# Optimization experiments

Measured on AMD Instinct MI355X. Metric: run time of the kernel, lower is better.

Reference implementation:

```python
import jax, jax.numpy as jnp
import numpy as np

B = 2048      # graphs per side
NPG = 40      # nodes per graph
N = B * NPG   # 81920 total nodes
E = 4 * N     # 327680 directed edges
IN_DIM = 74
H = 256
ADD = 8
GCR_LAYERS = 5
MLP1, MLP2 = 1024, 512


def setup_inputs() -> dict:
    key = jax.random.key(0)
    ks = jax.random.split(key, 24)
    n2g = jnp.repeat(jnp.arange(B, dtype=jnp.int32), NPG)
    s = 0.05
    d = {
        'cat_src': jax.random.randint(ks[0], (E,), 0, N, dtype=jnp.int32),
        'cat_dst': jax.random.randint(ks[1], (E,), 0, N, dtype=jnp.int32),
        'cat_n2g': n2g,
        'cat_x': jax.random.normal(ks[2], (N, IN_DIM), jnp.float32),
        'an_src': jax.random.randint(ks[3], (E,), 0, N, dtype=jnp.int32),
        'an_dst': jax.random.randint(ks[4], (E,), 0, N, dtype=jnp.int32),
        'an_n2g': n2g,
        'an_x': jax.random.normal(ks[5], (N, IN_DIM), jnp.float32),
        'add_features': jax.random.normal(ks[6], (B, ADD), jnp.float32),
        # shared GNN params (same module processes cation and anion)
        'W0': jax.random.normal(ks[7], (IN_DIM, H), jnp.float32) * s,
        'b0': jnp.zeros((H,), jnp.float32),
        'gcrW': jax.random.normal(ks[8], (GCR_LAYERS, 2, H, H), jnp.float32) * s,
        'gcrb': jnp.zeros((GCR_LAYERS, 2, H), jnp.float32),
        # MLP head: (2H + ADD) -> 1024 -> 512 -> 1
        'mW1': jax.random.normal(ks[9], (2 * H + ADD, MLP1), jnp.float32) * s,
        'mb1': jnp.zeros((MLP1,), jnp.float32),
        'mW2': jax.random.normal(ks[10], (MLP1, MLP2), jnp.float32) * s,
        'mb2': jnp.zeros((MLP2,), jnp.float32),
        'mW3': jax.random.normal(ks[11], (MLP2, 1), jnp.float32) * s,
        'mb3': jnp.zeros((1,), jnp.float32),
    }
    return d


def _graph_conv(src, dst, x, W, b):
    # DGL GraphConv, norm='both': out = D_in^{-1/2} A^T D_out^{-1/2} x W + b
    ones = jnp.ones(src.shape[0], x.dtype)
    deg_out = jnp.clip(jax.ops.segment_sum(ones, src, num_segments=N), 1.0)
    deg_in = jnp.clip(jax.ops.segment_sum(ones, dst, num_segments=N), 1.0)
    h = x * jax.lax.rsqrt(deg_out)[:, None]
    agg = jax.ops.segment_sum(h[src], dst, num_segments=N)  # [N, d]
    return (agg * jax.lax.rsqrt(deg_in)[:, None]) @ W + b


def _feat_extract(src, dst, n2g, x, W0, b0, gcrW, gcrb):
    h = _graph_conv(src, dst, x, W0, b0)  # no activation after first conv
    for i in range(GCR_LAYERS):
        o1 = _graph_conv(src, dst, h, gcrW[i, 0], gcrb[i, 0])
        o2 = _graph_conv(src, dst, jax.nn.relu(o1), gcrW[i, 1], gcrb[i, 1])
        h = jax.nn.relu(o2)  # res_connection = 0 -> plain replace
    # dgl.sum_nodes readout per graph
    return jax.ops.segment_sum(h, n2g, num_segments=B)  # [B, H]


def _leaky(x):
    return jnp.where(x > 0, x, 0.01 * x)  # nn.LeakyReLU default slope


def reference(cat_src, cat_dst, cat_n2g, cat_x, an_src, an_dst, an_n2g, an_x,
              add_features, W0, b0, gcrW, gcrb, mW1, mb1, mW2, mb2, mW3, mb3):
    cat_feat = _feat_extract(cat_src, cat_dst, cat_n2g, cat_x, W0, b0, gcrW, gcrb)
    an_feat = _feat_extract(an_src, an_dst, an_n2g, an_x, W0, b0, gcrW, gcrb)
    z = jnp.concatenate([cat_feat, an_feat, add_features], axis=1)  # [B, 2H+ADD]
    h = _leaky(z @ mW1 + mb1)
    h = _leaky(h @ mW2 + mb2)
    out = h @ mW3 + mb3  # [B, 1]
    return out.squeeze(-1)
```

## Files before the change

kernel.cpp:

```cpp
#include <hip/hip_runtime.h>


#define NN 81920
#define NN2 163840
#define NE 327680
#define NE2 655360
#define NB 2048
#define NB2 4096
#define H 256
#define INDIM 74
#define KPAD 128
#define ZK 576
#define DEGCAP 32
#define CPITCH 132

typedef unsigned short u16;
typedef __attribute__((ext_vector_type(8))) short short8;
typedef __attribute__((ext_vector_type(4))) float f32x4;

__device__ inline u16 f2b(float f) {
    unsigned u = __builtin_bit_cast(unsigned, f);
    u += 0x7fffu + ((u >> 16) & 1u);
    return (u16)(u >> 16);
}
__device__ inline float b2f(u16 b) {
    unsigned u = ((unsigned)b) << 16;
    return __builtin_bit_cast(float, u);
}
__device__ inline float blo(unsigned u) { return __builtin_bit_cast(float, u << 16); }
__device__ inline float bhi(unsigned u) { return __builtin_bit_cast(float, u & 0xffff0000u); }

__global__ void fill_kernel(const int* __restrict__ cs, const int* __restrict__ cd,
                            const int* __restrict__ as_, const int* __restrict__ ad,
                            int* __restrict__ dego, int* __restrict__ cnti,
                            int* __restrict__ bucket) {
    int e = blockIdx.x * 256 + threadIdx.x;
    if (e < NE2) {
        int s, d;
        if (e < NE) { s = cs[e]; d = cd[e]; }
        else        { s = as_[e - NE] + NN; d = ad[e - NE] + NN; }
        atomicAdd(&dego[s], 1);
        int p = atomicAdd(&cnti[d], 1);
        if (p < DEGCAP) bucket[(size_t)p * NN2 + d] = s;
    }
}

__global__ void rsqrt_kernel(const int* __restrict__ dego, const int* __restrict__ cnti,
                             float* __restrict__ rso, float* __restrict__ rsi) {
    int i = blockIdx.x * 256 + threadIdx.x;
    if (i < NN2) {
        rso[i] = rsqrtf((float)(dego[i] > 1 ? dego[i] : 1));
        rsi[i] = rsqrtf((float)(cnti[i] > 1 ? cnti[i] : 1));
    }
}

__global__ __launch_bounds__(256) void prescale_x_kernel(
        const float* __restrict__ cx, const float* __restrict__ ax,
        const float* __restrict__ rso, u16* __restrict__ xbp) {
    int t = threadIdx.x;
    int node = blockIdx.x * 4 + (t >> 6);
    int lane = t & 63;
    const float* x = (node < NN) ? (cx + (size_t)node * INDIM)
                                 : (ax + (size_t)(node - NN) * INDIM);
    float w = rso[node];
    int f0 = lane * 2, f1 = f0 + 1;
    u16 a = (f0 < INDIM) ? f2b(x[f0] * w) : (u16)0;
    u16 b = (f1 < INDIM) ? f2b(x[f1] * w) : (u16)0;
    ((unsigned*)xbp)[(size_t)node * 64 + lane] = a | ((unsigned)b << 16);
}

__global__ __launch_bounds__(256) void gather_x_kernel(
        const u16* __restrict__ xbp, const int* __restrict__ bucket,
        const int* __restrict__ cnti, const float* __restrict__ rsi,
        u16* __restrict__ out) {
    int node = blockIdx.x * 16 + (threadIdx.x >> 4);
    int fc = (threadIdx.x & 15) * 8;
    int deg = cnti[node]; if (deg > DEGCAP) deg = DEGCAP;
    const int* bk = bucket + node;
    float acc[8] = {};
    for (int base = 0; base < deg; base += 4) {
        int i0 = bk[(size_t)base * NN2];
        int i1 = (base + 1 < deg) ? bk[(size_t)(base + 1) * NN2] : i0;
        int i2 = (base + 2 < deg) ? bk[(size_t)(base + 2) * NN2] : i0;
        int i3 = (base + 3 < deg) ? bk[(size_t)(base + 3) * NN2] : i0;
        float m1 = (base + 1 < deg) ? 1.f : 0.f;
        float m2 = (base + 2 < deg) ? 1.f : 0.f;
        float m3 = (base + 3 < deg) ? 1.f : 0.f;
        uint4 v0 = *(const uint4*)(xbp + (size_t)i0 * KPAD + fc);
        uint4 v1 = *(const uint4*)(xbp + (size_t)i1 * KPAD + fc);
        uint4 v2 = *(const uint4*)(xbp + (size_t)i2 * KPAD + fc);
        uint4 v3 = *(const uint4*)(xbp + (size_t)i3 * KPAD + fc);
        acc[0] += blo(v0.x) + m1 * blo(v1.x) + m2 * blo(v2.x) + m3 * blo(v3.x);
        acc[1] += bhi(v0.x) + m1 * bhi(v1.x) + m2 * bhi(v2.x) + m3 * bhi(v3.x);
        acc[2] += blo(v0.y) + m1 * blo(v1.y) + m2 * blo(v2.y) + m3 * blo(v3.y);
        acc[3] += bhi(v0.y) + m1 * bhi(v1.y) + m2 * bhi(v2.y) + m3 * bhi(v3.y);
        acc[4] += blo(v0.z) + m1 * blo(v1.z) + m2 * blo(v2.z) + m3 * blo(v3.z);
        acc[5] += bhi(v0.z) + m1 * bhi(v1.z) + m2 * bhi(v2.z) + m3 * bhi(v3.z);
        acc[6] += blo(v0.w) + m1 * blo(v1.w) + m2 * blo(v2.w) + m3 * blo(v3.w);
        acc[7] += bhi(v0.w) + m1 * bhi(v1.w) + m2 * bhi(v2.w) + m3 * bhi(v3.w);
    }
    float ri = rsi[node];
    u16 o[8];
#pragma unroll
    for (int i = 0; i < 8; ++i) o[i] = f2b(acc[i] * ri);
    uint4 ov;
    ov.x = o[0] | ((unsigned)o[1] << 16);
    ov.y = o[2] | ((unsigned)o[3] << 16);
    ov.z = o[4] | ((unsigned)o[5] << 16);
    ov.w = o[6] | ((unsigned)o[7] << 16);
    *(uint4*)(out + (size_t)node * KPAD + fc) = ov;
}

__global__ __launch_bounds__(256) void gather_h_kernel(
        const u16* __restrict__ h, const int* __restrict__ bucket,
        const int* __restrict__ cnti, const float* __restrict__ rso,
        const float* __restrict__ rsi, u16* __restrict__ out) {
    int node = blockIdx.x * 8 + (threadIdx.x >> 5);
    int fc = (threadIdx.x & 31) * 8;
    int deg = cnti[node]; if (deg > DEGCAP) deg = DEGCAP;
    const int* bk = bucket + node;
    float acc[8] = {};
    for (int base = 0; base < deg; base += 4) {
        int i0 = bk[(size_t)base * NN2];
        int i1 = (base + 1 < deg) ? bk[(size_t)(base + 1) * NN2] : i0;
        int i2 = (base + 2 < deg) ? bk[(size_t)(base + 2) * NN2] : i0;
        int i3 = (base + 3 < deg) ? bk[(size_t)(base + 3) * NN2] : i0;
        float w0 = rso[i0];
        float w1 = (base + 1 < deg) ? rso[i1] : 0.f;
        float w2 = (base + 2 < deg) ? rso[i2] : 0.f;
        float w3 = (base + 3 < deg) ? rso[i3] : 0.f;
        uint4 v0 = *(const uint4*)(h + (size_t)i0 * H + fc);
        uint4 v1 = *(const uint4*)(h + (size_t)i1 * H + fc);
        uint4 v2 = *(const uint4*)(h + (size_t)i2 * H + fc);
        uint4 v3 = *(const uint4*)(h + (size_t)i3 * H + fc);
        acc[0] += blo(v0.x) * w0 + blo(v1.x) * w1 + blo(v2.x) * w2 + blo(v3.x) * w3;
        acc[1] += bhi(v0.x) * w0 + bhi(v1.x) * w1 + bhi(v2.x) * w2 + bhi(v3.x) * w3;
        acc[2] += blo(v0.y) * w0 + blo(v1.y) * w1 + blo(v2.y) * w2 + blo(v3.y) * w3;
        acc[3] += bhi(v0.y) * w0 + bhi(v1.y) * w1 + bhi(v2.y) * w2 + bhi(v3.y) * w3;
        acc[4] += blo(v0.z) * w0 + blo(v1.z) * w1 + blo(v2.z) * w2 + blo(v3.z) * w3;
        acc[5] += bhi(v0.z) * w0 + bhi(v1.z) * w1 + bhi(v2.z) * w2 + bhi(v3.z) * w3;
        acc[6] += blo(v0.w) * w0 + blo(v1.w) * w1 + blo(v2.w) * w2 + blo(v3.w) * w3;
        acc[7] += bhi(v0.w) * w0 + bhi(v1.w) * w1 + bhi(v2.w) * w2 + bhi(v3.w) * w3;
    }
    float ri = rsi[node];
    u16 o[8];
#pragma unroll
    for (int i = 0; i < 8; ++i) o[i] = f2b(acc[i] * ri);
    uint4 ov;
    ov.x = o[0] | ((unsigned)o[1] << 16);
    ov.y = o[2] | ((unsigned)o[3] << 16);
    ov.z = o[4] | ((unsigned)o[5] << 16);
    ov.w = o[6] | ((unsigned)o[7] << 16);
    *(uint4*)(out + (size_t)node * H + fc) = ov;
}

__global__ void prep_w0_kernel(const float* __restrict__ W0, u16* __restrict__ Wt0) {
    int i = blockIdx.x * 256 + threadIdx.x;
    int n = i >> 7, k = i & 127;
    float v = (k < INDIM) ? W0[(size_t)k * H + n] : 0.f;
    Wt0[i] = f2b(v);
}

__global__ void prep_gcr_kernel(const float* __restrict__ W, u16* __restrict__ Wt) {
    int i = blockIdx.x * 256 + threadIdx.x;
    int l = blockIdx.y;
    int n = i >> 8, k = i & 255;
    Wt[(size_t)l * 65536 + i] = f2b(W[(size_t)l * 65536 + (size_t)k * H + n]);
}

__global__ void prep_w1_kernel(const float* __restrict__ W, u16* __restrict__ Wt) {
    int i = blockIdx.x * 256 + threadIdx.x;
    if (i >= 1024 * ZK) return;
    int n = i / ZK, k = i - n * ZK;
    float v = (k < 520) ? W[(size_t)k * 1024 + n] : 0.f;
    Wt[i] = f2b(v);
}

__global__ void prep_w2_kernel(const float* __restrict__ W, u16* __restrict__ Wt) {
    int i = blockIdx.x * 256 + threadIdx.x;
    int n = i >> 10, k = i & 1023;
    Wt[i] = f2b(W[(size_t)k * 512 + n]);
}

__device__ inline void ldg_lds16(const u16* g, u16* l) {
    __builtin_amdgcn_global_load_lds(
        (const __attribute__((address_space(1))) unsigned int*)g,
        (__attribute__((address_space(3))) unsigned int*)l, 16, 0, 0);
}
__device__ inline float actf(float v, int act) {
    if (act == 1) return fmaxf(v, 0.f);
    if (act == 2) return (v > 0.f) ? v : 0.01f * v;
    return v;
}

__global__ __launch_bounds__(256) void gemm_mfma_kernel(
        const u16* __restrict__ A, int lda,
        const u16* __restrict__ Bt, int ldb,
        const float* __restrict__ bias, u16* __restrict__ C, int ldc,
        int Kiters, int act) {
    __shared__ __align__(16) u16 smem[128 * CPITCH];
    u16* As = smem;
    u16* Bs = smem + 8192;
    int t = threadIdx.x;
    int wave = t >> 6, lane = t & 63;
    int wr = wave >> 1, wc = wave & 1;
    int row0 = blockIdx.y * 128, col0 = blockIdx.x * 128;

    int sr = t >> 3;
    int ksrc = (((t & 7) ^ (sr & 7))) * 8;
    const u16* Ag[4];
    const u16* Bg[4];
#pragma unroll
    for (int c = 0; c < 4; ++c) {
        Ag[c] = A + (size_t)(row0 + c * 32 + sr) * lda + ksrc;
        Bg[c] = Bt + (size_t)(col0 + c * 32 + sr) * ldb + ksrc;
    }
    u16* AsW = As + wave * 512;
    u16* BsW = Bs + wave * 512;

    f32x4 acc[4][4] = {};
    int mrow = lane & 15;
    int q = lane >> 4;

    for (int kt = 0; kt < Kiters; ++kt) {
#pragma unroll
        for (int c = 0; c < 4; ++c) ldg_lds16(Ag[c], AsW + c * 2048);
#pragma unroll
        for (int c = 0; c < 4; ++c) ldg_lds16(Bg[c], BsW + c * 2048);
        __syncthreads();
#pragma unroll
        for (int kk = 0; kk < 2; ++kk) {
            short8 a[4], b[4];
#pragma unroll
            for (int mt = 0; mt < 4; ++mt) {
                int row = wr * 64 + mt * 16 + mrow;
                int seg = (kk * 4 + q) ^ (row & 7);
                a[mt] = *(const short8*)(As + row * 64 + seg * 8);
            }
#pragma unroll
            for (int nt = 0; nt < 4; ++nt) {
                int row = wc * 64 + nt * 16 + mrow;
                int seg = (kk * 4 + q) ^ (row & 7);
                b[nt] = *(const short8*)(Bs + row * 64 + seg * 8);
            }
#pragma unroll
            for (int mt = 0; mt < 4; ++mt)
#pragma unroll
                for (int nt = 0; nt < 4; ++nt)
                    acc[mt][nt] = __builtin_amdgcn_mfma_f32_16x16x32_bf16(
                        a[mt], b[nt], acc[mt][nt], 0, 0, 0);
        }
        __syncthreads();
#pragma unroll
        for (int c = 0; c < 4; ++c) { Ag[c] += 64; Bg[c] += 64; }
    }

#pragma unroll
    for (int mt = 0; mt < 4; ++mt) {
        int rl = wr * 64 + mt * 16 + q * 4;
#pragma unroll
        for (int nt = 0; nt < 4; ++nt) {
            int cl = wc * 64 + nt * 16 + mrow;
            float bv = bias[col0 + cl];
#pragma unroll
            for (int qq = 0; qq < 4; ++qq) {
                float v = actf(acc[mt][nt][qq] + bv, act);
                smem[(size_t)(rl + qq) * CPITCH + cl] = f2b(v);
            }
        }
    }
    __syncthreads();
    int rr = t >> 4;
    int seg = t & 15;
#pragma unroll
    for (int pass = 0; pass < 8; ++pass) {
        int row = pass * 16 + rr;
        uint4 val = *(const uint4*)(smem + (size_t)row * CPITCH + seg * 8);
        *(uint4*)(C + (size_t)(row0 + row) * ldc + col0 + seg * 8) = val;
    }
}

__global__ __launch_bounds__(256) void pool_kernel(const u16* __restrict__ h,
                                                   u16* __restrict__ z) {
    int g = blockIdx.x, f = threadIdx.x;
    float acc = 0.f;
    const u16* base = h + (size_t)g * 40 * H + f;
#pragma unroll
    for (int j = 0; j < 40; ++j) acc += b2f(base[j * H]);
    int zrow = g & (NB - 1);
    int zoff = (g >> 11) * H;
    z[(size_t)zrow * ZK + zoff + f] = f2b(acc);
}

__global__ void copy_add_kernel(const float* __restrict__ add, u16* __restrict__ z) {
    int i = blockIdx.x * 256 + threadIdx.x;
    if (i < NB * 8) {
        int g = i >> 3, a = i & 7;
        z[(size_t)g * ZK + 512 + a] = f2b(add[i]);
    }
}

__global__ void gemv_out_kernel(const u16* __restrict__ A, const float* __restrict__ w,
                                const float* __restrict__ b, float* __restrict__ out, int K) {
    int wave = threadIdx.x >> 6;
    int lane = threadIdx.x & 63;
    int row = blockIdx.x * 4 + wave;
    float acc = 0.f;
    for (int k = lane; k < K; k += 64) acc += b2f(A[(size_t)row * K + k]) * w[k];
#pragma unroll
    for (int off = 32; off > 0; off >>= 1) acc += __shfl_down(acc, off, 64);
    if (lane == 0) out[row] = acc + b[0];
}

extern "C" void kernel_launch(void* const* d_in, const int* in_sizes, int n_in,
                              void* d_out, int out_size, void* d_ws, size_t ws_size,
                              hipStream_t stream) {
    const int*   cat_src = (const int*)d_in[0];
    const int*   cat_dst = (const int*)d_in[1];
    const float* cat_x   = (const float*)d_in[3];
    const int*   an_src  = (const int*)d_in[4];
    const int*   an_dst  = (const int*)d_in[5];
    const float* an_x    = (const float*)d_in[7];
    const float* add_f   = (const float*)d_in[8];
    const float* W0      = (const float*)d_in[9];
    const float* b0      = (const float*)d_in[10];
    const float* gcrW    = (const float*)d_in[11];
    const float* gcrb    = (const float*)d_in[12];
    const float* mW1     = (const float*)d_in[13];
    const float* mb1     = (const float*)d_in[14];
    const float* mW2     = (const float*)d_in[15];
    const float* mb2     = (const float*)d_in[16];
    const float* mW3     = (const float*)d_in[17];
    const float* mb3     = (const float*)d_in[18];
    float* out = (float*)d_out;

    char* p = (char*)d_ws;
    auto alloc = [&](size_t bytes) -> void* {
        void* rp = (void*)p;
        p += (bytes + 255) & ~(size_t)255;
        return rp;
    };
    int*   dego   = (int*)alloc((size_t)NN2 * 4);
    int*   cnti   = (int*)alloc((size_t)NN2 * 4);
    int*   bucket = (int*)alloc((size_t)NN2 * DEGCAP * 4);
    float* rso    = (float*)alloc((size_t)NN2 * 4);
    float* rsi    = (float*)alloc((size_t)NN2 * 4);
    u16*   hA     = (u16*)alloc((size_t)NN2 * H * 2);
    u16*   hB     = (u16*)alloc((size_t)NN2 * H * 2);
    u16*   Wt0    = (u16*)alloc((size_t)H * KPAD * 2);
    u16*   Wtg    = (u16*)alloc((size_t)10 * H * H * 2);
    u16*   Wt1    = (u16*)alloc((size_t)1024 * ZK * 2);
    u16*   Wt2    = (u16*)alloc((size_t)512 * 1024 * 2);
    u16*   zb     = (u16*)alloc((size_t)NB * ZK * 2);
    u16*   m1b    = (u16*)alloc((size_t)NB * 1024 * 2);
    u16*   m2b    = (u16*)alloc((size_t)NB * 512 * 2);
    u16*   xbp    = hA;
    u16*   aggx   = hB;
    (void)ws_size; (void)in_sizes; (void)n_in; (void)out_size;

    prep_w0_kernel<<<(H * KPAD) / 256, 256, 0, stream>>>(W0, Wt0);
    prep_gcr_kernel<<<dim3(H * H / 256, 10), 256, 0, stream>>>(gcrW, Wtg);
    prep_w1_kernel<<<(1024 * ZK + 255) / 256, 256, 0, stream>>>(mW1, Wt1);
    prep_w2_kernel<<<(512 * 1024) / 256, 256, 0, stream>>>(mW2, Wt2);
    hipMemsetAsync(zb, 0, (size_t)NB * ZK * 2, stream);
    hipMemsetAsync(dego, 0, (size_t)NN2 * 4, stream);
    hipMemsetAsync(cnti, 0, (size_t)NN2 * 4, stream);

    fill_kernel<<<NE2 / 256, 256, 0, stream>>>(cat_src, cat_dst, an_src, an_dst,
                                               dego, cnti, bucket);
    rsqrt_kernel<<<NN2 / 256, 256, 0, stream>>>(dego, cnti, rso, rsi);

    prescale_x_kernel<<<NN2 / 4, 256, 0, stream>>>(cat_x, an_x, rso, xbp);
    gather_x_kernel<<<NN2 / 16, 256, 0, stream>>>(xbp, bucket, cnti, rsi, aggx);
    gemm_mfma_kernel<<<dim3(H / 128, NN2 / 128), 256, 0, stream>>>(
        aggx, KPAD, Wt0, KPAD, b0, hA, H, KPAD / 64, 0);

    for (int l = 0; l < 10; ++l) {
        gather_h_kernel<<<NN2 / 8, 256, 0, stream>>>(hA, bucket, cnti, rso, rsi, hB);
        gemm_mfma_kernel<<<dim3(H / 128, NN2 / 128), 256, 0, stream>>>(
            hB, H, Wtg + (size_t)l * H * H, H, gcrb + (size_t)l * H, hA, H,
            H / 64, 1);
    }
    pool_kernel<<<NB2, 256, 0, stream>>>(hA, zb);
    copy_add_kernel<<<(NB * 8 + 255) / 256, 256, 0, stream>>>(add_f, zb);

    gemm_mfma_kernel<<<dim3(1024 / 128, NB / 128), 256, 0, stream>>>(
        zb, ZK, Wt1, ZK, mb1, m1b, 1024, ZK / 64, 2);
    gemm_mfma_kernel<<<dim3(512 / 128, NB / 128), 256, 0, stream>>>(
        m1b, 1024, Wt2, 1024, mb2, m2b, 512, 1024 / 64, 2);
    gemv_out_kernel<<<NB / 4, 256, 0, stream>>>(m2b, mW3, mb3, out, 512);
}
```

Baseline: 1.490 ms.

## Fuse neighbor gather with MFMA GEMM into a single graph-conv kernel

Replaces the separate gather kernels and the GEMM in each graph-conv layer with one templated kernel. Each block gathers and normalizes 128 nodes' aggregated features straight into swizzled LDS, then multiplies them by streamed weight tiles with bf16 MFMA and writes bias-plus-activation output. This removes the global write and re-read of the aggregated intermediate and half the kernel launches. In exchange it uses a large LDS footprint that caps occupancy at two blocks per CU. The latency-bound gather phase is also serialized with the matmul inside each block, and ping-pong buffers are reassigned.

```diff
diff --git a/kernel.cpp b/kernel.cpp
--- a/kernel.cpp
+++ b/kernel.cpp
@@ -69,91 +69,6 @@
     ((unsigned*)xbp)[(size_t)node * 64 + lane] = a | ((unsigned)b << 16);
 }
 
-__global__ __launch_bounds__(256) void gather_x_kernel(
-        const u16* __restrict__ xbp, const int* __restrict__ bucket,
-        const int* __restrict__ cnti, const float* __restrict__ rsi,
-        u16* __restrict__ out) {
-    int node = blockIdx.x * 16 + (threadIdx.x >> 4);
-    int fc = (threadIdx.x & 15) * 8;
-    int deg = cnti[node]; if (deg > DEGCAP) deg = DEGCAP;
-    const int* bk = bucket + node;
-    float acc[8] = {};
-    for (int base = 0; base < deg; base += 4) {
-        int i0 = bk[(size_t)base * NN2];
-        int i1 = (base + 1 < deg) ? bk[(size_t)(base + 1) * NN2] : i0;
-        int i2 = (base + 2 < deg) ? bk[(size_t)(base + 2) * NN2] : i0;
-        int i3 = (base + 3 < deg) ? bk[(size_t)(base + 3) * NN2] : i0;
-        float m1 = (base + 1 < deg) ? 1.f : 0.f;
-        float m2 = (base + 2 < deg) ? 1.f : 0.f;
-        float m3 = (base + 3 < deg) ? 1.f : 0.f;
-        uint4 v0 = *(const uint4*)(xbp + (size_t)i0 * KPAD + fc);
-        uint4 v1 = *(const uint4*)(xbp + (size_t)i1 * KPAD + fc);
-        uint4 v2 = *(const uint4*)(xbp + (size_t)i2 * KPAD + fc);
-        uint4 v3 = *(const uint4*)(xbp + (size_t)i3 * KPAD + fc);
-        acc[0] += blo(v0.x) + m1 * blo(v1.x) + m2 * blo(v2.x) + m3 * blo(v3.x);
-        acc[1] += bhi(v0.x) + m1 * bhi(v1.x) + m2 * bhi(v2.x) + m3 * bhi(v3.x);
-        acc[2] += blo(v0.y) + m1 * blo(v1.y) + m2 * blo(v2.y) + m3 * blo(v3.y);
-        acc[3] += bhi(v0.y) + m1 * bhi(v1.y) + m2 * bhi(v2.y) + m3 * bhi(v3.y);
-        acc[4] += blo(v0.z) + m1 * blo(v1.z) + m2 * blo(v2.z) + m3 * blo(v3.z);
-        acc[5] += bhi(v0.z) + m1 * bhi(v1.z) + m2 * bhi(v2.z) + m3 * bhi(v3.z);
-        acc[6] += blo(v0.w) + m1 * blo(v1.w) + m2 * blo(v2.w) + m3 * blo(v3.w);
-        acc[7] += bhi(v0.w) + m1 * bhi(v1.w) + m2 * bhi(v2.w) + m3 * bhi(v3.w);
-    }
-    float ri = rsi[node];
-    u16 o[8];
-#pragma unroll
-    for (int i = 0; i < 8; ++i) o[i] = f2b(acc[i] * ri);
-    uint4 ov;
-    ov.x = o[0] | ((unsigned)o[1] << 16);
-    ov.y = o[2] | ((unsigned)o[3] << 16);
-    ov.z = o[4] | ((unsigned)o[5] << 16);
-    ov.w = o[6] | ((unsigned)o[7] << 16);
-    *(uint4*)(out + (size_t)node * KPAD + fc) = ov;
-}
-
-__global__ __launch_bounds__(256) void gather_h_kernel(
-        const u16* __restrict__ h, const int* __restrict__ bucket,
-        const int* __restrict__ cnti, const float* __restrict__ rso,
-        const float* __restrict__ rsi, u16* __restrict__ out) {
-    int node = blockIdx.x * 8 + (threadIdx.x >> 5);
-    int fc = (threadIdx.x & 31) * 8;
-    int deg = cnti[node]; if (deg > DEGCAP) deg = DEGCAP;
-    const int* bk = bucket + node;
-    float acc[8] = {};
-    for (int base = 0; base < deg; base += 4) {
-        int i0 = bk[(size_t)base * NN2];
-        int i1 = (base + 1 < deg) ? bk[(size_t)(base + 1) * NN2] : i0;
-        int i2 = (base + 2 < deg) ? bk[(size_t)(base + 2) * NN2] : i0;
-        int i3 = (base + 3 < deg) ? bk[(size_t)(base + 3) * NN2] : i0;
-        float w0 = rso[i0];
-        float w1 = (base + 1 < deg) ? rso[i1] : 0.f;
-        float w2 = (base + 2 < deg) ? rso[i2] : 0.f;
-        float w3 = (base + 3 < deg) ? rso[i3] : 0.f;
-        uint4 v0 = *(const uint4*)(h + (size_t)i0 * H + fc);
-        uint4 v1 = *(const uint4*)(h + (size_t)i1 * H + fc);
-        uint4 v2 = *(const uint4*)(h + (size_t)i2 * H + fc);
-        uint4 v3 = *(const uint4*)(h + (size_t)i3 * H + fc);
-        acc[0] += blo(v0.x) * w0 + blo(v1.x) * w1 + blo(v2.x) * w2 + blo(v3.x) * w3;
-        acc[1] += bhi(v0.x) * w0 + bhi(v1.x) * w1 + bhi(v2.x) * w2 + bhi(v3.x) * w3;
-        acc[2] += blo(v0.y) * w0 + blo(v1.y) * w1 + blo(v2.y) * w2 + blo(v3.y) * w3;
-        acc[3] += bhi(v0.y) * w0 + bhi(v1.y) * w1 + bhi(v2.y) * w2 + bhi(v3.y) * w3;
-        acc[4] += blo(v0.z) * w0 + blo(v1.z) * w1 + blo(v2.z) * w2 + blo(v3.z) * w3;
-        acc[5] += bhi(v0.z) * w0 + bhi(v1.z) * w1 + bhi(v2.z) * w2 + bhi(v3.z) * w3;
-        acc[6] += blo(v0.w) * w0 + blo(v1.w) * w1 + blo(v2.w) * w2 + blo(v3.w) * w3;
-        acc[7] += bhi(v0.w) * w0 + bhi(v1.w) * w1 + bhi(v2.w) * w2 + bhi(v3.w) * w3;
-    }
-    float ri = rsi[node];
-    u16 o[8];
-#pragma unroll
-    for (int i = 0; i < 8; ++i) o[i] = f2b(acc[i] * ri);
-    uint4 ov;
-    ov.x = o[0] | ((unsigned)o[1] << 16);
-    ov.y = o[2] | ((unsigned)o[3] << 16);
-    ov.z = o[4] | ((unsigned)o[5] << 16);
-    ov.w = o[6] | ((unsigned)o[7] << 16);
-    *(uint4*)(out + (size_t)node * H + fc) = ov;
-}
-
 __global__ void prep_w0_kernel(const float* __restrict__ W0, u16* __restrict__ Wt0) {
     int i = blockIdx.x * 256 + threadIdx.x;
     int n = i >> 7, k = i & 127;
@@ -191,6 +106,146 @@
     if (act == 1) return fmaxf(v, 0.f);
     if (act == 2) return (v > 0.f) ? v : 0.01f * v;
     return v;
+}
+
+template <int KD, bool RSO>
+__global__ __launch_bounds__(256, 2) void fused_conv_kernel(
+        const u16* __restrict__ hIn, const int* __restrict__ bucket,
+        const int* __restrict__ cnti, const float* __restrict__ rso,
+        const float* __restrict__ rsi, const u16* __restrict__ Bt,
+        const float* __restrict__ bias, u16* __restrict__ hOut,
+        int act) {
+    constexpr int NCH = KD / 8;
+    constexpr int KT  = KD / 64;
+    __shared__ __align__(16) u16 smem[128 * KD + 128 * 64];
+    u16* As = smem;
+    u16* Bs = smem + 128 * KD;
+
+    int t = threadIdx.x;
+    int n0 = blockIdx.x * 128;
+    int wave = t >> 6, lane = t & 63;
+    int wr = wave >> 1, wc = wave & 1;
+    int mrow = lane & 15, q = lane >> 4;
+
+    for (int i = 0; i < (128 * NCH) / 256; ++i) {
+        int gid = i * 256 + t;
+        int nl = gid / NCH;
+        int ch = gid % NCH;
+        int node = n0 + nl;
+        int deg = cnti[node]; if (deg > DEGCAP) deg = DEGCAP;
+        const int* bk = bucket + node;
+        int fc = ch * 8;
+        float acc[8] = {};
+        for (int base = 0; base < deg; base += 4) {
+            int i0 = bk[(size_t)base * NN2];
+            int i1 = (base + 1 < deg) ? bk[(size_t)(base + 1) * NN2] : i0;
+            int i2 = (base + 2 < deg) ? bk[(size_t)(base + 2) * NN2] : i0;
+            int i3 = (base + 3 < deg) ? bk[(size_t)(base + 3) * NN2] : i0;
+            float w0, w1, w2, w3;
+            if (RSO) {
+                w0 = rso[i0];
+                w1 = (base + 1 < deg) ? rso[i1] : 0.f;
+                w2 = (base + 2 < deg) ? rso[i2] : 0.f;
+                w3 = (base + 3 < deg) ? rso[i3] : 0.f;
+            } else {
+                w0 = 1.f;
+                w1 = (base + 1 < deg) ? 1.f : 0.f;
+                w2 = (base + 2 < deg) ? 1.f : 0.f;
+                w3 = (base + 3 < deg) ? 1.f : 0.f;
+            }
+            uint4 v0 = *(const uint4*)(hIn + (size_t)i0 * KD + fc);
+            uint4 v1 = *(const uint4*)(hIn + (size_t)i1 * KD + fc);
+            uint4 v2 = *(const uint4*)(hIn + (size_t)i2 * KD + fc);
+            uint4 v3 = *(const uint4*)(hIn + (size_t)i3 * KD + fc);
+            acc[0] += blo(v0.x) * w0 + blo(v1.x) * w1 + blo(v2.x) * w2 + blo(v3.x) * w3;
+            acc[1] += bhi(v0.x) * w0 + bhi(v1.x) * w1 + bhi(v2.x) * w2 + bhi(v3.x) * w3;
+            acc[2] += blo(v0.y) * w0 + blo(v1.y) * w1 + blo(v2.y) * w2 + blo(v3.y) * w3;
+            acc[3] += bhi(v0.y) * w0 + bhi(v1.y) * w1 + bhi(v2.y) * w2 + bhi(v3.y) * w3;
+            acc[4] += blo(v0.z) * w0 + blo(v1.z) * w1 + blo(v2.z) * w2 + blo(v3.z) * w3;
+            acc[5] += bhi(v0.z) * w0 + bhi(v1.z) * w1 + bhi(v2.z) * w2 + bhi(v3.z) * w3;
+            acc[6] += blo(v0.w) * w0 + blo(v1.w) * w1 + blo(v2.w) * w2 + blo(v3.w) * w3;
+            acc[7] += bhi(v0.w) * w0 + bhi(v1.w) * w1 + bhi(v2.w) * w2 + bhi(v3.w) * w3;
+        }
+        float ri = rsi[node];
+        u16 o[8];
+#pragma unroll
+        for (int j = 0; j < 8; ++j) o[j] = f2b(acc[j] * ri);
+        uint4 ov;
+        ov.x = o[0] | ((unsigned)o[1] << 16);
+        ov.y = o[2] | ((unsigned)o[3] << 16);
+        ov.z = o[4] | ((unsigned)o[5] << 16);
+        ov.w = o[6] | ((unsigned)o[7] << 16);
+        int kt = ch >> 3, seg = ch & 7;
+        *(uint4*)(As + (size_t)kt * 8192 + nl * 64 + ((seg ^ (nl & 7)) * 8)) = ov;
+    }
+    __syncthreads();
+
+    int sr = t >> 3;
+    int ksseg = ((t & 7) ^ (sr & 7)) * 8;
+    u16* BsW = Bs + wave * 512;
+
+    f32x4 acc[4][8] = {};
+    for (int kt = 0; kt < KT; ++kt) {
+        const u16* Ak = As + kt * 8192;
+#pragma unroll
+        for (int nh = 0; nh < 2; ++nh) {
+#pragma unroll
+            for (int c = 0; c < 4; ++c)
+                ldg_lds16(Bt + (size_t)(nh * 128 + c * 32 + sr) * KD + kt * 64 + ksseg,
+                          BsW + c * 2048);
+            __syncthreads();
+#pragma unroll
+            for (int kk = 0; kk < 2; ++kk) {
+                short8 a[4], b[4];
+#pragma unroll
+                for (int mt = 0; mt < 4; ++mt) {
+                    int row = wr * 64 + mt * 16 + mrow;
+                    int seg = (kk * 4 + q) ^ (row & 7);
+                    a[mt] = *(const short8*)(Ak + row * 64 + seg * 8);
+                }
+#pragma unroll
+                for (int nt = 0; nt < 4; ++nt) {
+                    int row = wc * 64 + nt * 16 + mrow;
+                    int seg = (kk * 4 + q) ^ (row & 7);
+                    b[nt] = *(const short8*)(Bs + row * 64 + seg * 8);
+                }
+#pragma unroll
+                for (int mt = 0; mt < 4; ++mt)
+#pragma unroll
+                    for (int nt = 0; nt < 4; ++nt)
+                        acc[mt][nh * 4 + nt] = __builtin_amdgcn_mfma_f32_16x16x32_bf16(
+                            a[mt], b[nt], acc[mt][nh * 4 + nt], 0, 0, 0);
+            }
+            __syncthreads();
+        }
+    }
+
+#pragma unroll
+    for (int nh = 0; nh < 2; ++nh) {
+#pragma unroll
+        for (int mt = 0; mt < 4; ++mt) {
+            int rl = wr * 64 + mt * 16 + q * 4;
+#pragma unroll
+            for (int nt = 0; nt < 4; ++nt) {
+                int cl = wc * 64 + nt * 16 + mrow;
+                float bv = bias[nh * 128 + cl];
+#pragma unroll
+                for (int qq = 0; qq < 4; ++qq) {
+                    float v = actf(acc[mt][nh * 4 + nt][qq] + bv, act);
+                    smem[(size_t)(rl + qq) * CPITCH + cl] = f2b(v);
+                }
+            }
+        }
+        __syncthreads();
+        int rr = t >> 4, sg = t & 15;
+#pragma unroll
+        for (int pass = 0; pass < 8; ++pass) {
+            int row = pass * 16 + rr;
+            uint4 val = *(const uint4*)(smem + (size_t)row * CPITCH + sg * 8);
+            *(uint4*)(hOut + (size_t)(n0 + row) * 256 + nh * 128 + sg * 8) = val;
+        }
+        __syncthreads();
+    }
 }
 
 __global__ __launch_bounds__(256) void gemm_mfma_kernel(
@@ -355,7 +410,6 @@
     u16*   m1b    = (u16*)alloc((size_t)NB * 1024 * 2);
     u16*   m2b    = (u16*)alloc((size_t)NB * 512 * 2);
     u16*   xbp    = hA;
-    u16*   aggx   = hB;
     (void)ws_size; (void)in_sizes; (void)n_in; (void)out_size;
 
     prep_w0_kernel<<<(H * KPAD) / 256, 256, 0, stream>>>(W0, Wt0);
@@ -371,17 +425,17 @@
     rsqrt_kernel<<<NN2 / 256, 256, 0, stream>>>(dego, cnti, rso, rsi);
 
     prescale_x_kernel<<<NN2 / 4, 256, 0, stream>>>(cat_x, an_x, rso, xbp);
-    gather_x_kernel<<<NN2 / 16, 256, 0, stream>>>(xbp, bucket, cnti, rsi, aggx);
-    gemm_mfma_kernel<<<dim3(H / 128, NN2 / 128), 256, 0, stream>>>(
-        aggx, KPAD, Wt0, KPAD, b0, hA, H, KPAD / 64, 0);
+    fused_conv_kernel<KPAD, false><<<NN2 / 128, 256, 0, stream>>>(
+        xbp, bucket, cnti, rso, rsi, Wt0, b0, hB, 0);
 
     for (int l = 0; l < 10; ++l) {
-        gather_h_kernel<<<NN2 / 8, 256, 0, stream>>>(hA, bucket, cnti, rso, rsi, hB);
-        gemm_mfma_kernel<<<dim3(H / 128, NN2 / 128), 256, 0, stream>>>(
-            hB, H, Wtg + (size_t)l * H * H, H, gcrb + (size_t)l * H, hA, H,
-            H / 64, 1);
-    }
-    pool_kernel<<<NB2, 256, 0, stream>>>(hA, zb);
+        const u16* hin = (l & 1) ? hA : hB;
+        u16*       hout = (l & 1) ? hB : hA;
+        fused_conv_kernel<H, true><<<NN2 / 128, 256, 0, stream>>>(
+            hin, bucket, cnti, rso, rsi, Wtg + (size_t)l * H * H,
+            gcrb + (size_t)l * H, hout, 1);
+    }
+    pool_kernel<<<NB2, 256, 0, stream>>>(hB, zb);
     copy_add_kernel<<<(NB * 8 + 255) / 256, 256, 0, stream>>>(add_f, zb);
 
     gemm_mfma_kernel<<<dim3(1024 / 128, NB / 128), 256, 0, stream>>>(
```

New measurement: 1.971 ms. 32.3% more time.
